# Kernel optimization log

Measured on AMD Instinct MI355X. Metric: run time of the kernel, lower is better.

Reference implementation:

```python
import jax, jax.numpy as jnp
import numpy as np

K, S, P = 3, 2, 2  # kernel_size, stride, padding (dilation=1)


def _unfold(xp, k, s, oh, ow):
    """Extract k*k strided patches from a padded array.

    xp: (..., Hp, Wp) -> (..., k*k, oh, ow), window-position ordering (kh, kw)
    matching torch.nn.Unfold (channel-major handled by caller).
    """
    return jnp.stack(
        [xp[..., i:i + s * (oh - 1) + 1:s, j:j + s * (ow - 1) + 1:s]
         for i in range(K) for j in range(K)],
        axis=-3,
    )


def setup_inputs() -> dict:
    key = jax.random.key(0)
    x = jax.random.normal(key, (8, 256, 128, 128), dtype=jnp.float32)
    return {"x": x}


def reference(x):
    b, c, h, w = x.shape
    oh = (h - K + 2 * P) // S + 1
    ow = (w - K + 2 * P) // S + 1

    # channel-wise L2 norm, computed BEFORE unfolding (padding contributes 0 either way)
    n = jnp.sqrt(jnp.sum(x * x, axis=1))            # (b, h, w)
    n_pad = jnp.pad(n, ((0, 0), (P, P), (P, P)))
    n_patch = _unfold(n_pad, K, S, oh, ow)          # (b, k*k, oh, ow)
    # weighting_fn = softmax over the k*k window positions (torch dim=1 of unfolded norm)
    wts = jax.nn.softmax(n_patch, axis=1)           # (b, k*k, oh, ow)

    x_pad = jnp.pad(x, ((0, 0), (0, 0), (P, P), (P, P)))
    x_patch = _unfold(x_pad, K, S, oh, ow)          # (b, c, k*k, oh, ow)

    # weighted sum over window positions
    return jnp.sum(wts[:, None] * x_patch, axis=2)  # (b, c, oh, ow)
```

## Files before the change

kernel.cpp:

```cpp
#include <hip/hip_runtime.h>
#include <math.h>

#define BATCH 8
#define CH    256
#define H     128
#define W     128
#define HW    (H * W)
#define OH    65
#define OW    65
#define NPIX  (OH * OW)
#define CGRP  32

__global__ __launch_bounds__(256) void norm_kernel(const float4* __restrict__ x4,
                                                   float4* __restrict__ n4) {
    __shared__ float4 part[4][64];
    const int lane = threadIdx.x & 63;
    const int wv   = threadIdx.x >> 6;
    const int q    = blockIdx.x * 64 + lane;
    const int b    = (q * 4) >> 14;
    const int qin  = q - b * (HW / 4);

    const float4* p = x4 + (size_t)(b * CH + wv * 64) * (HW / 4) + qin;
    float4 acc = {0.f, 0.f, 0.f, 0.f};
    #pragma unroll 8
    for (int c = 0; c < 64; ++c) {
        float4 v = p[(size_t)c * (HW / 4)];
        acc.x += v.x * v.x; acc.y += v.y * v.y;
        acc.z += v.z * v.z; acc.w += v.w * v.w;
    }
    part[wv][lane] = acc;
    __syncthreads();
    if (wv == 0) {
        float4 a0 = part[0][lane], a1 = part[1][lane];
        float4 a2 = part[2][lane], a3 = part[3][lane];
        float4 r;
        r.x = sqrtf(a0.x + a1.x + a2.x + a3.x);
        r.y = sqrtf(a0.y + a1.y + a2.y + a3.y);
        r.z = sqrtf(a0.z + a1.z + a2.z + a3.z);
        r.w = sqrtf(a0.w + a1.w + a2.w + a3.w);
        n4[q] = r;
    }
}

__global__ __launch_bounds__(256) void pool_kernel(const float* __restrict__ x,
                                                   const float* __restrict__ n,
                                                   float* __restrict__ out) {
    int p = blockIdx.x * blockDim.x + threadIdx.x;
    if (p >= NPIX) return;
    const int b  = blockIdx.y;
    const int cg = blockIdx.z;
    const int oh = p / OW;
    const int ow = p - oh * OW;
    const int iw0 = ow * 2 - 2;

    const float* nb = n + b * HW;

    float nv[9];
    bool  val[9];
    float m = 0.0f;
    #pragma unroll
    for (int kh = 0; kh < 3; ++kh) {
        int ih = oh * 2 + kh - 2;
        bool vh = (unsigned)ih < (unsigned)H;
        #pragma unroll
        for (int kw = 0; kw < 3; ++kw) {
            int iw = iw0 + kw;
            int k = kh * 3 + kw;
            bool v = vh && ((unsigned)iw < (unsigned)W);
            val[k] = v;
            nv[k]  = v ? nb[ih * W + iw] : 0.0f;
            m = fmaxf(m, nv[k]);
        }
    }
    float denom = 0.0f;
    float wts[9];
    #pragma unroll
    for (int k = 0; k < 9; ++k) {
        float e = __expf(nv[k] - m);
        denom += e;
        wts[k] = val[k] ? e : 0.0f;
    }
    float inv = 1.0f / denom;
    #pragma unroll
    for (int k = 0; k < 9; ++k) wts[k] *= inv;

    int off2[3], offs[3];
    const int iwa = iw0 < 0 ? 0 : iw0;
    const int iwc = (iw0 + 2) > (W - 1) ? (W - 1) : (iw0 + 2);
    #pragma unroll
    for (int r = 0; r < 3; ++r) {
        int ih = oh * 2 + r - 2;
        int ihc = ih < 0 ? 0 : (ih > H - 1 ? H - 1 : ih);
        off2[r] = ihc * W + iwa;
        offs[r] = ihc * W + iwc;
    }

    const float* xb = x + (size_t)(b * CH + cg * CGRP) * HW;
    float*       ob = out + (size_t)(b * CH + cg * CGRP) * NPIX + p;

    #pragma unroll 4
    for (int c = 0; c < CGRP; ++c) {
        const float* xc = xb + (size_t)c * HW;
        float acc = 0.f;
        #pragma unroll
        for (int r = 0; r < 3; ++r) {
            float2 v2 = *(const float2*)(xc + off2[r]);
            float  vs = xc[offs[r]];
            acc += wts[r * 3 + 0] * v2.x + wts[r * 3 + 1] * v2.y + wts[r * 3 + 2] * vs;
        }
        ob[(size_t)c * NPIX] = acc;
    }
}

extern "C" void kernel_launch(void* const* d_in, const int* in_sizes, int n_in,
                              void* d_out, int out_size, void* d_ws, size_t ws_size,
                              hipStream_t stream) {
    const float* x = (const float*)d_in[0];
    float* out = (float*)d_out;
    float* nbuf = (float*)d_ws;

    norm_kernel<<<512, 256, 0, stream>>>((const float4*)x, (float4*)nbuf);

    dim3 grid((NPIX + 255) / 256, BATCH, CH / CGRP);
    pool_kernel<<<grid, 256, 0, stream>>>(x, nbuf, out);
}
```

Before: 233.0 us.

## Pipeline norm and pooling across batches in fused per-batch stage launches

Replaces the two whole-tensor kernels with a single stage kernel launched once per batch. Each launch computes the channel norm for batch b+1 in some blocks while other blocks do the weighted pooling for batch b. The aim is to overlap the two phases and to reuse batch data while it is still in cache, instead of streaming the whole input twice. Pooling channel groups shrink from 32 to 8 with the channel loop fully unrolled, and the norm uses 32-channel slices across 8 wavefront groups. This adds nine launches and smaller per-launch grids, which cost launch overhead and some tail inefficiency.

```diff
diff --git a/kernel.cpp b/kernel.cpp
--- a/kernel.cpp
+++ b/kernel.cpp
@@ -9,46 +9,50 @@
 #define OH    65
 #define OW    65
 #define NPIX  (OH * OW)
-#define CGRP  32
+#define CGRP  8
+#define PBLK  17
+#define POOL_BLOCKS (PBLK * (CH / CGRP))
+#define NORM_BLOCKS 128
 
-__global__ __launch_bounds__(256) void norm_kernel(const float4* __restrict__ x4,
-                                                   float4* __restrict__ n4) {
-    __shared__ float4 part[4][64];
-    const int lane = threadIdx.x & 63;
-    const int wv   = threadIdx.x >> 6;
-    const int q    = blockIdx.x * 64 + lane;
-    const int b    = (q * 4) >> 14;
-    const int qin  = q - b * (HW / 4);
-
-    const float4* p = x4 + (size_t)(b * CH + wv * 64) * (HW / 4) + qin;
+__device__ __forceinline__ void norm_body(const float4* __restrict__ x4,
+                                          float4* __restrict__ n4,
+                                          int b, int blk, int tid) {
+    __shared__ float4 part[8][32];
+    const int q  = tid & 31;
+    const int ck = tid >> 5;
+    const int qg = blk * 32 + q;
+    const float4* p = x4 + (size_t)(b * CH + ck * 32) * (HW / 4) + qg;
     float4 acc = {0.f, 0.f, 0.f, 0.f};
-    #pragma unroll 8
-    for (int c = 0; c < 64; ++c) {
+    #pragma unroll 16
+    for (int c = 0; c < 32; ++c) {
         float4 v = p[(size_t)c * (HW / 4)];
         acc.x += v.x * v.x; acc.y += v.y * v.y;
         acc.z += v.z * v.z; acc.w += v.w * v.w;
     }
-    part[wv][lane] = acc;
+    part[ck][q] = acc;
     __syncthreads();
-    if (wv == 0) {
-        float4 a0 = part[0][lane], a1 = part[1][lane];
-        float4 a2 = part[2][lane], a3 = part[3][lane];
+    if (tid < 32) {
+        float4 s = part[0][tid];
+        #pragma unroll
+        for (int k = 1; k < 8; ++k) {
+            float4 a = part[k][tid];
+            s.x += a.x; s.y += a.y; s.z += a.z; s.w += a.w;
+        }
         float4 r;
-        r.x = sqrtf(a0.x + a1.x + a2.x + a3.x);
-        r.y = sqrtf(a0.y + a1.y + a2.y + a3.y);
-        r.z = sqrtf(a0.z + a1.z + a2.z + a3.z);
-        r.w = sqrtf(a0.w + a1.w + a2.w + a3.w);
-        n4[q] = r;
+        r.x = sqrtf(s.x); r.y = sqrtf(s.y);
+        r.z = sqrtf(s.z); r.w = sqrtf(s.w);
+        n4[(size_t)b * (HW / 4) + blk * 32 + tid] = r;
     }
 }
 
-__global__ __launch_bounds__(256) void pool_kernel(const float* __restrict__ x,
-                                                   const float* __restrict__ n,
-                                                   float* __restrict__ out) {
-    int p = blockIdx.x * blockDim.x + threadIdx.x;
+__device__ __forceinline__ void pool_body(const float* __restrict__ x,
+                                          const float* __restrict__ n,
+                                          float* __restrict__ out,
+                                          int b, int pid) {
+    const int cg = pid / PBLK;
+    const int pt = pid - cg * PBLK;
+    const int p  = pt * 256 + threadIdx.x;
     if (p >= NPIX) return;
-    const int b  = blockIdx.y;
-    const int cg = blockIdx.z;
     const int oh = p / OW;
     const int ow = p - oh * OW;
     const int iw0 = ow * 2 - 2;
@@ -98,7 +102,7 @@
     const float* xb = x + (size_t)(b * CH + cg * CGRP) * HW;
     float*       ob = out + (size_t)(b * CH + cg * CGRP) * NPIX + p;
 
-    #pragma unroll 4
+    #pragma unroll
     for (int c = 0; c < CGRP; ++c) {
         const float* xc = xb + (size_t)c * HW;
         float acc = 0.f;
@@ -112,6 +116,17 @@
     }
 }
 
+__global__ __launch_bounds__(256)
+void stage_kernel(const float* __restrict__ x, float* __restrict__ nbuf,
+                  float* __restrict__ out, int b_norm, int b_pool,
+                  int n_norm_blocks) {
+    if ((int)blockIdx.x < n_norm_blocks) {
+        norm_body((const float4*)x, (float4*)nbuf, b_norm, blockIdx.x, threadIdx.x);
+    } else {
+        pool_body(x, nbuf, out, b_pool, blockIdx.x - n_norm_blocks);
+    }
+}
+
 extern "C" void kernel_launch(void* const* d_in, const int* in_sizes, int n_in,
                               void* d_out, int out_size, void* d_ws, size_t ws_size,
                               hipStream_t stream) {
@@ -119,8 +134,10 @@
     float* out = (float*)d_out;
     float* nbuf = (float*)d_ws;
 
-    norm_kernel<<<512, 256, 0, stream>>>((const float4*)x, (float4*)nbuf);
-
-    dim3 grid((NPIX + 255) / 256, BATCH, CH / CGRP);
-    pool_kernel<<<grid, 256, 0, stream>>>(x, nbuf, out);
+    stage_kernel<<<NORM_BLOCKS, 256, 0, stream>>>(x, nbuf, out, 0, 0, NORM_BLOCKS);
+    for (int b = 0; b < BATCH - 1; ++b) {
+        stage_kernel<<<NORM_BLOCKS + POOL_BLOCKS, 256, 0, stream>>>(
+            x, nbuf, out, b + 1, b, NORM_BLOCKS);
+    }
+    stage_kernel<<<POOL_BLOCKS, 256, 0, stream>>>(x, nbuf, out, 0, BATCH - 1, 0);
 }
```

Result: slower. 246.3 us (+5.7%).

## Fuse norm and softmax pooling into one kernel per output row

Applied to the files above, without the earlier changes.

Replaces the separate norm kernel and pooling kernel with a single kernel in which each block handles one (batch, output row). Each block computes the channel norms for the three input rows it needs, reduces them in shared memory, builds the softmax weights per output column, and then computes all channels for that row. This removes the norm buffer round-trip and one launch, but each input row is read twice per block and rows shared between adjacent output rows are read by two blocks. The grid also drops to 520 large blocks.

```diff
diff --git a/kernel.cpp b/kernel.cpp
--- a/kernel.cpp
+++ b/kernel.cpp
@@ -9,106 +9,118 @@
 #define OH    65
 #define OW    65
 #define NPIX  (OH * OW)
-#define CGRP  32
+#define TPB   512
+#define WAVES 8
+#define CPW   (CH / WAVES)
+#define TASKS (CPW * OW)
+#define ITERS ((TASKS + 63) / 64)
 
-__global__ __launch_bounds__(256) void norm_kernel(const float4* __restrict__ x4,
-                                                   float4* __restrict__ n4) {
-    __shared__ float4 part[4][64];
-    const int lane = threadIdx.x & 63;
-    const int wv   = threadIdx.x >> 6;
-    const int q    = blockIdx.x * 64 + lane;
-    const int b    = (q * 4) >> 14;
-    const int qin  = q - b * (HW / 4);
+__global__ __launch_bounds__(TPB) void fused_kernel(const float* __restrict__ x,
+                                                    float* __restrict__ out) {
+    const int bx   = blockIdx.x;
+    const int b    = bx / OH;
+    const int oh   = bx - b * OH;
+    const int tid  = threadIdx.x;
+    const int lane = tid & 63;
+    const int wv   = tid >> 6;
 
-    const float4* p = x4 + (size_t)(b * CH + wv * 64) * (HW / 4) + qin;
-    float4 acc = {0.f, 0.f, 0.f, 0.f};
-    #pragma unroll 8
-    for (int c = 0; c < 64; ++c) {
-        float4 v = p[(size_t)c * (HW / 4)];
-        acc.x += v.x * v.x; acc.y += v.y * v.y;
-        acc.z += v.z * v.z; acc.w += v.w * v.w;
-    }
-    part[wv][lane] = acc;
-    __syncthreads();
-    if (wv == 0) {
-        float4 a0 = part[0][lane], a1 = part[1][lane];
-        float4 a2 = part[2][lane], a3 = part[3][lane];
-        float4 r;
-        r.x = sqrtf(a0.x + a1.x + a2.x + a3.x);
-        r.y = sqrtf(a0.y + a1.y + a2.y + a3.y);
-        r.z = sqrtf(a0.z + a1.z + a2.z + a3.z);
-        r.w = sqrtf(a0.w + a1.w + a2.w + a3.w);
-        n4[q] = r;
-    }
-}
-
-__global__ __launch_bounds__(256) void pool_kernel(const float* __restrict__ x,
-                                                   const float* __restrict__ n,
-                                                   float* __restrict__ out) {
-    int p = blockIdx.x * blockDim.x + threadIdx.x;
-    if (p >= NPIX) return;
-    const int b  = blockIdx.y;
-    const int cg = blockIdx.z;
-    const int oh = p / OW;
-    const int ow = p - oh * OW;
-    const int iw0 = ow * 2 - 2;
-
-    const float* nb = n + b * HW;
-
-    float nv[9];
-    bool  val[9];
-    float m = 0.0f;
-    #pragma unroll
-    for (int kh = 0; kh < 3; ++kh) {
-        int ih = oh * 2 + kh - 2;
-        bool vh = (unsigned)ih < (unsigned)H;
-        #pragma unroll
-        for (int kw = 0; kw < 3; ++kw) {
-            int iw = iw0 + kw;
-            int k = kh * 3 + kw;
-            bool v = vh && ((unsigned)iw < (unsigned)W);
-            val[k] = v;
-            nv[k]  = v ? nb[ih * W + iw] : 0.0f;
-            m = fmaxf(m, nv[k]);
-        }
-    }
-    float denom = 0.0f;
-    float wts[9];
-    #pragma unroll
-    for (int k = 0; k < 9; ++k) {
-        float e = __expf(nv[k] - m);
-        denom += e;
-        wts[k] = val[k] ? e : 0.0f;
-    }
-    float inv = 1.0f / denom;
-    #pragma unroll
-    for (int k = 0; k < 9; ++k) wts[k] *= inv;
-
-    int off2[3], offs[3];
-    const int iwa = iw0 < 0 ? 0 : iw0;
-    const int iwc = (iw0 + 2) > (W - 1) ? (W - 1) : (iw0 + 2);
+    int  rowc[3];
+    bool rv[3];
     #pragma unroll
     for (int r = 0; r < 3; ++r) {
         int ih = oh * 2 + r - 2;
-        int ihc = ih < 0 ? 0 : (ih > H - 1 ? H - 1 : ih);
-        off2[r] = ihc * W + iwa;
-        offs[r] = ihc * W + iwc;
+        rv[r]   = (unsigned)ih < (unsigned)H;
+        rowc[r] = ih < 0 ? 0 : (ih > H - 1 ? H - 1 : ih);
     }
 
-    const float* xb = x + (size_t)(b * CH + cg * CGRP) * HW;
-    float*       ob = out + (size_t)(b * CH + cg * CGRP) * NPIX + p;
+    __shared__ float part[WAVES][3][W];
+    __shared__ float nrm[3][W];
+    __shared__ float wls[OH][11];
 
+    const float* xw = x + (size_t)(b * CH + wv * CPW) * HW;
+    float2 a0 = {0.f, 0.f}, a1 = {0.f, 0.f}, a2 = {0.f, 0.f};
     #pragma unroll 4
-    for (int c = 0; c < CGRP; ++c) {
-        const float* xc = xb + (size_t)c * HW;
-        float acc = 0.f;
+    for (int c = 0; c < CPW; ++c) {
+        const float* xp = xw + (size_t)c * HW;
+        float2 v0 = *(const float2*)(xp + rowc[0] * W + 2 * lane);
+        float2 v1 = *(const float2*)(xp + rowc[1] * W + 2 * lane);
+        float2 v2 = *(const float2*)(xp + rowc[2] * W + 2 * lane);
+        a0.x += v0.x * v0.x; a0.y += v0.y * v0.y;
+        a1.x += v1.x * v1.x; a1.y += v1.y * v1.y;
+        a2.x += v2.x * v2.x; a2.y += v2.y * v2.y;
+    }
+    *(float2*)&part[wv][0][2 * lane] = a0;
+    *(float2*)&part[wv][1][2 * lane] = a1;
+    *(float2*)&part[wv][2][2 * lane] = a2;
+    __syncthreads();
+
+    if (tid < 3 * W) {
+        int r = tid >> 7, col = tid & (W - 1);
+        float s = 0.f;
         #pragma unroll
-        for (int r = 0; r < 3; ++r) {
-            float2 v2 = *(const float2*)(xc + off2[r]);
-            float  vs = xc[offs[r]];
-            acc += wts[r * 3 + 0] * v2.x + wts[r * 3 + 1] * v2.y + wts[r * 3 + 2] * vs;
+        for (int w = 0; w < WAVES; ++w) s += part[w][r][col];
+        nrm[r][col] = sqrtf(s);
+    }
+    __syncthreads();
+
+    if (tid < OH) {
+        const int ow  = tid;
+        const int iw0 = ow * 2 - 2;
+        float nv[9];
+        bool  val[9];
+        float m = 0.0f;
+        #pragma unroll
+        for (int kh = 0; kh < 3; ++kh) {
+            bool vh = rv[kh];
+            #pragma unroll
+            for (int kw = 0; kw < 3; ++kw) {
+                int iw = iw0 + kw;
+                int k  = kh * 3 + kw;
+                bool v = vh && ((unsigned)iw < (unsigned)W);
+                val[k] = v;
+                nv[k]  = v ? nrm[kh][iw] : 0.0f;
+                m = fmaxf(m, nv[k]);
+            }
         }
-        ob[(size_t)c * NPIX] = acc;
+        float denom = 0.0f, wt[9];
+        #pragma unroll
+        for (int k = 0; k < 9; ++k) {
+            float e = __expf(nv[k] - m);
+            denom += e;
+            wt[k] = val[k] ? e : 0.0f;
+        }
+        float inv = 1.0f / denom;
+        #pragma unroll
+        for (int k = 0; k < 9; ++k) wls[ow][k] = wt[k] * inv;
+    }
+    __syncthreads();
+
+    float* ob = out + (size_t)(b * CH + wv * CPW) * NPIX + (size_t)oh * OW;
+    #pragma unroll 2
+    for (int it = 0; it < ITERS; ++it) {
+        int id = it * 64 + lane;
+        if (id < TASKS) {
+            int c  = id / OW;
+            int ow = id - c * OW;
+            int iw0 = ow * 2 - 2;
+            int iwa = iw0 < 0 ? 0 : iw0;
+            int iwc = (iw0 + 2) > (W - 1) ? (W - 1) : (iw0 + 2);
+            float w0 = wls[ow][0], w1 = wls[ow][1], w2 = wls[ow][2];
+            float w3 = wls[ow][3], w4 = wls[ow][4], w5 = wls[ow][5];
+            float w6 = wls[ow][6], w7 = wls[ow][7], w8 = wls[ow][8];
+            const float* xc = xw + (size_t)c * HW;
+            const float* r0 = xc + rowc[0] * W;
+            const float* r1 = xc + rowc[1] * W;
+            const float* r2 = xc + rowc[2] * W;
+            float2 p0 = *(const float2*)(r0 + iwa);
+            float2 p1 = *(const float2*)(r1 + iwa);
+            float2 p2 = *(const float2*)(r2 + iwa);
+            float  s0 = r0[iwc], s1 = r1[iwc], s2 = r2[iwc];
+            float acc = w0 * p0.x + w1 * p0.y + w2 * s0
+                      + w3 * p1.x + w4 * p1.y + w5 * s1
+                      + w6 * p2.x + w7 * p2.y + w8 * s2;
+            ob[(size_t)c * NPIX + ow] = acc;
+        }
     }
 }
 
@@ -117,10 +129,6 @@
                               hipStream_t stream) {
     const float* x = (const float*)d_in[0];
     float* out = (float*)d_out;
-    float* nbuf = (float*)d_ws;
-
-    norm_kernel<<<512, 256, 0, stream>>>((const float4*)x, (float4*)nbuf);
-
-    dim3 grid((NPIX + 255) / 256, BATCH, CH / CGRP);
-    pool_kernel<<<grid, 256, 0, stream>>>(x, nbuf, out);
+    (void)d_ws; (void)ws_size;
+    fused_kernel<<<BATCH * OH, TPB, 0, stream>>>(x, out);
 }
```

New measurement: 251.8 us. 8.1% more time.

## Tile pool kernel by output rows with shared-memory softmax weights

Applied to the files above, without the earlier changes.

The norm kernel now uses 512 threads, each covering 32 channels and two float4 columns, and reduces eight wave partials in shared memory. The pool kernel is restructured so each block handles an 8-output-row tile for 8 channels. It loads the needed norm rows into shared memory, computes softmax weights once per tile into LDS and reuses them across channels. The aim is to raise parallelism and cut redundant global norm loads. In exchange, softmax weights are recomputed for every group of 8 channels (32 times per pixel), and the per-element index math uses divisions.

```diff
diff --git a/kernel.cpp b/kernel.cpp
--- a/kernel.cpp
+++ b/kernel.cpp
@@ -9,106 +9,130 @@
 #define OH    65
 #define OW    65
 #define NPIX  (OH * OW)
-#define CGRP  32
 
-__global__ __launch_bounds__(256) void norm_kernel(const float4* __restrict__ x4,
-                                                   float4* __restrict__ n4) {
-    __shared__ float4 part[4][64];
+#define NTILE   512
+#define K1_TPB  512
+#define K1_CPW  32
+
+__global__ __launch_bounds__(K1_TPB) void norm_kernel(const float4* __restrict__ x4,
+                                                      float* __restrict__ nrm) {
+    const int tile = blockIdx.x;
+    const int b    = tile >> 5;
+    const int t    = tile & 31;
     const int lane = threadIdx.x & 63;
     const int wv   = threadIdx.x >> 6;
-    const int q    = blockIdx.x * 64 + lane;
-    const int b    = (q * 4) >> 14;
-    const int qin  = q - b * (HW / 4);
 
-    const float4* p = x4 + (size_t)(b * CH + wv * 64) * (HW / 4) + qin;
-    float4 acc = {0.f, 0.f, 0.f, 0.f};
+    const float4* p = x4 + (size_t)(b * CH + wv * K1_CPW) * (HW / 4)
+                         + t * (NTILE / 4) + lane;
+    float4 a0 = {0.f, 0.f, 0.f, 0.f}, a1 = {0.f, 0.f, 0.f, 0.f};
     #pragma unroll 8
-    for (int c = 0; c < 64; ++c) {
-        float4 v = p[(size_t)c * (HW / 4)];
-        acc.x += v.x * v.x; acc.y += v.y * v.y;
-        acc.z += v.z * v.z; acc.w += v.w * v.w;
+    for (int c = 0; c < K1_CPW; ++c) {
+        float4 v0 = p[(size_t)c * (HW / 4)];
+        float4 v1 = p[(size_t)c * (HW / 4) + 64];
+        a0.x += v0.x * v0.x; a0.y += v0.y * v0.y;
+        a0.z += v0.z * v0.z; a0.w += v0.w * v0.w;
+        a1.x += v1.x * v1.x; a1.y += v1.y * v1.y;
+        a1.z += v1.z * v1.z; a1.w += v1.w * v1.w;
     }
-    part[wv][lane] = acc;
+    __shared__ float part[8][NTILE];
+    ((float4*)part[wv])[lane]      = a0;
+    ((float4*)part[wv])[64 + lane] = a1;
     __syncthreads();
-    if (wv == 0) {
-        float4 a0 = part[0][lane], a1 = part[1][lane];
-        float4 a2 = part[2][lane], a3 = part[3][lane];
-        float4 r;
-        r.x = sqrtf(a0.x + a1.x + a2.x + a3.x);
-        r.y = sqrtf(a0.y + a1.y + a2.y + a3.y);
-        r.z = sqrtf(a0.z + a1.z + a2.z + a3.z);
-        r.w = sqrtf(a0.w + a1.w + a2.w + a3.w);
-        n4[q] = r;
-    }
+
+    float s = 0.f;
+    #pragma unroll
+    for (int w = 0; w < 8; ++w) s += part[w][threadIdx.x];
+    nrm[(size_t)b * HW + t * NTILE + threadIdx.x] = sqrtf(s);
 }
 
-__global__ __launch_bounds__(256) void pool_kernel(const float* __restrict__ x,
-                                                   const float* __restrict__ n,
-                                                   float* __restrict__ out) {
-    int p = blockIdx.x * blockDim.x + threadIdx.x;
-    if (p >= NPIX) return;
-    const int b  = blockIdx.y;
-    const int cg = blockIdx.z;
-    const int oh = p / OW;
-    const int ow = p - oh * OW;
-    const int iw0 = ow * 2 - 2;
+#define R       8
+#define CPB     8
+#define K2_TPB  256
+#define NT      ((OH + R - 1) / R)
+#define NROWS   (2 * R + 1)
+#define WSETS   (R * OW)
 
-    const float* nb = n + b * HW;
+__global__ __launch_bounds__(K2_TPB) void pool_kernel(const float* __restrict__ x,
+                                                      const float* __restrict__ nrm,
+                                                      float* __restrict__ out) {
+    const int ohT = blockIdx.x;
+    const int cg  = blockIdx.y;
+    const int b   = blockIdx.z;
+    const int oh0 = ohT * R;
+    const int tid = threadIdx.x;
 
-    float nv[9];
-    bool  val[9];
-    float m = 0.0f;
-    #pragma unroll
-    for (int kh = 0; kh < 3; ++kh) {
-        int ih = oh * 2 + kh - 2;
-        bool vh = (unsigned)ih < (unsigned)H;
-        #pragma unroll
-        for (int kw = 0; kw < 3; ++kw) {
-            int iw = iw0 + kw;
-            int k = kh * 3 + kw;
-            bool v = vh && ((unsigned)iw < (unsigned)W);
-            val[k] = v;
-            nv[k]  = v ? nb[ih * W + iw] : 0.0f;
-            m = fmaxf(m, nv[k]);
+    __shared__ float ns[NROWS][W];
+    __shared__ float wls[WSETS][9];
+
+    for (int id = tid; id < NROWS * W; id += K2_TPB) {
+        int r = id >> 7, col = id & (W - 1);
+        int ih  = oh0 * 2 - 2 + r;
+        int ihc = ih < 0 ? 0 : (ih > H - 1 ? H - 1 : ih);
+        ns[r][col] = nrm[(size_t)b * HW + ihc * W + col];
+    }
+    __syncthreads();
+
+    for (int id = tid; id < WSETS; id += K2_TPB) {
+        int ohl = id / OW;
+        int ow  = id - ohl * OW;
+        int oh  = oh0 + ohl;
+        if (oh < OH) {
+            int iw0 = ow * 2 - 2;
+            float nv[9]; bool val[9]; float m = 0.0f;
+            #pragma unroll
+            for (int kh = 0; kh < 3; ++kh) {
+                int ih = oh * 2 + kh - 2;
+                bool vh = (unsigned)ih < (unsigned)H;
+                int rL = 2 * ohl + kh;
+                #pragma unroll
+                for (int kw = 0; kw < 3; ++kw) {
+                    int iw = iw0 + kw;
+                    int k  = kh * 3 + kw;
+                    bool v = vh && ((unsigned)iw < (unsigned)W);
+                    val[k] = v;
+                    nv[k]  = v ? ns[rL][iw] : 0.0f;
+                    m = fmaxf(m, nv[k]);
+                }
+            }
+            float denom = 0.0f, wt[9];
+            #pragma unroll
+            for (int k = 0; k < 9; ++k) {
+                float e = __expf(nv[k] - m);
+                denom += e;
+                wt[k] = val[k] ? e : 0.0f;
+            }
+            float inv = 1.0f / denom;
+            #pragma unroll
+            for (int k = 0; k < 9; ++k) wls[id][k] = wt[k] * inv;
         }
     }
-    float denom = 0.0f;
-    float wts[9];
-    #pragma unroll
-    for (int k = 0; k < 9; ++k) {
-        float e = __expf(nv[k] - m);
-        denom += e;
-        wts[k] = val[k] ? e : 0.0f;
-    }
-    float inv = 1.0f / denom;
-    #pragma unroll
-    for (int k = 0; k < 9; ++k) wts[k] *= inv;
+    __syncthreads();
 
-    int off2[3], offs[3];
-    const int iwa = iw0 < 0 ? 0 : iw0;
-    const int iwc = (iw0 + 2) > (W - 1) ? (W - 1) : (iw0 + 2);
-    #pragma unroll
-    for (int r = 0; r < 3; ++r) {
-        int ih = oh * 2 + r - 2;
-        int ihc = ih < 0 ? 0 : (ih > H - 1 ? H - 1 : ih);
-        off2[r] = ihc * W + iwa;
-        offs[r] = ihc * W + iwc;
-    }
-
-    const float* xb = x + (size_t)(b * CH + cg * CGRP) * HW;
-    float*       ob = out + (size_t)(b * CH + cg * CGRP) * NPIX + p;
-
-    #pragma unroll 4
-    for (int c = 0; c < CGRP; ++c) {
-        const float* xc = xb + (size_t)c * HW;
+    const float* xg = x + (size_t)(b * CH + cg * CPB) * HW;
+    float*       og = out + (size_t)(b * CH + cg * CPB) * NPIX;
+    for (int id = tid; id < CPB * WSETS; id += K2_TPB) {
+        int c   = id / WSETS;
+        int rem = id - c * WSETS;
+        int ohl = rem / OW;
+        int ow  = rem - ohl * OW;
+        int oh  = oh0 + ohl;
+        if (oh >= OH) continue;
+        int iw0 = ow * 2 - 2;
+        int iwa = iw0 < 0 ? 0 : iw0;
+        int iwc = (iw0 + 2) > (W - 1) ? (W - 1) : (iw0 + 2);
+        const float* xc = xg + (size_t)c * HW;
         float acc = 0.f;
         #pragma unroll
         for (int r = 0; r < 3; ++r) {
-            float2 v2 = *(const float2*)(xc + off2[r]);
-            float  vs = xc[offs[r]];
-            acc += wts[r * 3 + 0] * v2.x + wts[r * 3 + 1] * v2.y + wts[r * 3 + 2] * vs;
+            int ih  = oh * 2 + r - 2;
+            int ihc = ih < 0 ? 0 : (ih > H - 1 ? H - 1 : ih);
+            float2 v2 = *(const float2*)(xc + ihc * W + iwa);
+            float  vs = xc[ihc * W + iwc];
+            acc += wls[rem][r * 3 + 0] * v2.x
+                 + wls[rem][r * 3 + 1] * v2.y
+                 + wls[rem][r * 3 + 2] * vs;
         }
-        ob[(size_t)c * NPIX] = acc;
+        og[(size_t)c * NPIX + oh * OW + ow] = acc;
     }
 }
 
@@ -116,11 +140,11 @@
                               void* d_out, int out_size, void* d_ws, size_t ws_size,
                               hipStream_t stream) {
     const float* x = (const float*)d_in[0];
-    float* out = (float*)d_out;
+    float* out  = (float*)d_out;
     float* nbuf = (float*)d_ws;
 
-    norm_kernel<<<512, 256, 0, stream>>>((const float4*)x, (float4*)nbuf);
+    norm_kernel<<<BATCH * (HW / NTILE), K1_TPB, 0, stream>>>((const float4*)x, nbuf);
 
-    dim3 grid((NPIX + 255) / 256, BATCH, CH / CGRP);
-    pool_kernel<<<grid, 256, 0, stream>>>(x, nbuf, out);
+    dim3 grid(NT, CH / CPB, BATCH);
+    pool_kernel<<<grid, K2_TPB, 0, stream>>>(x, nbuf, out);
 }
```

Measured after the change: 232.6 us. No clear change (-0.2%).
